# Kernel optimization log

Measured on AMD Instinct MI355X. Metric: run time of the kernel, lower is better.

## Reference

```python
import jax, jax.numpy as jnp
import numpy as np

# Dims: B=1, S=2048, D=1024, L=4 blocks, INNER=2*D=2048, NH=4 heads (DH=512),
# conv K=4, qkv blocksize BS=4 (NB=512 block-diagonal blocks).

def _ln(x, w, eps=1e-5):
    mu = x.mean(-1, keepdims=True)
    var = x.var(-1, keepdims=True)
    return (x - mu) * jax.lax.rsqrt(var + eps) * w


def setup_inputs() -> dict:
    key = jax.random.key(0)
    B, S, D = 1, 2048, 1024
    L, NH, K, BS = 4, 4, 4, 4
    INNER = 2 * D
    NB = INNER // BS
    ks = iter(jax.random.split(key, 40))
    rn = lambda *sh: jax.random.normal(next(ks), sh, jnp.float32) * 0.02
    return dict(
        tokens_batch=jax.random.normal(next(ks), (B, S, D), jnp.float32),
        ln_w=jnp.ones((L, D), jnp.float32),
        up_w=rn(L, 2 * INNER, D),
        conv_w=rn(L, INNER, K),
        conv_b=jnp.zeros((L, INNER), jnp.float32),
        q_w=rn(L, NB, BS, BS),
        k_w=rn(L, NB, BS, BS),
        v_w=rn(L, NB, BS, BS),
        ig_w=rn(L, NH, 3 * INNER),
        ig_b=jnp.zeros((L, NH), jnp.float32),
        fg_w=rn(L, NH, 3 * INNER),
        fg_b=jnp.tile(jnp.linspace(3.0, 6.0, NH, dtype=jnp.float32), (L, 1)),
        skip=jnp.ones((L, INNER), jnp.float32),
        onorm_w=jnp.ones((L, INNER), jnp.float32),
        down_w=rn(L, D, INNER),
        post_w=jnp.ones((D,), jnp.float32),
        lat_w=rn(32 * 32, D), lat_b=jnp.zeros((32 * 32,), jnp.float32),
        r1_w=rn(D, D), r1_b=jnp.zeros((D,), jnp.float32),
        r2_w=rn(1, D), r2_b=jnp.zeros((1,), jnp.float32),
        t1_w=rn(D, D), t1_b=jnp.zeros((D,), jnp.float32),
        t2_w=rn(1, D), t2_b=jnp.zeros((1,), jnp.float32),
    )


def reference(tokens_batch, ln_w, up_w, conv_w, conv_b, q_w, k_w, v_w,
              ig_w, ig_b, fg_w, fg_b, skip, onorm_w, down_w, post_w,
              lat_w, lat_b, r1_w, r1_b, r2_w, r2_b, t1_w, t1_b, t2_w, t2_b):
    B, S, D = tokens_batch.shape
    L, INNER, K = conv_w.shape
    NH = ig_w.shape[1]
    DH = INNER // NH
    NB, BS = q_w.shape[1], q_w.shape[2]
    mask = jnp.tril(jnp.ones((S, S), bool))
    x = tokens_batch
    for l in range(L):
        xn = _ln(x, ln_w[l])                                  # pre-LN (weight only)
        up = jnp.einsum('bsd,ed->bse', xn, up_w[l])           # (B,S,2*INNER)
        xm, z = up[..., :INNER], up[..., INNER:]
        # causal depthwise conv1d + swish
        xp = jnp.pad(xm, ((0, 0), (K - 1, 0), (0, 0)))
        xc = conv_b[l] + sum(xp[:, k:k + S, :] * conv_w[l, :, k] for k in range(K))
        xc = jax.nn.silu(xc)
        # block-diagonal (headwise) q/k/v projections
        def headwise(inp, w):
            return jnp.einsum('bsnd,nod->bsno', inp.reshape(B, S, NB, BS), w).reshape(B, S, INNER)
        q = headwise(xc, q_w[l]); kk = headwise(xc, k_w[l]); v = headwise(xm, v_w[l])
        gin = jnp.concatenate([q, kk, v], axis=-1)            # (B,S,3*INNER)
        ig = (jnp.einsum('bse,he->bsh', gin, ig_w[l]) + ig_b[l]).transpose(0, 2, 1)  # (B,NH,S)
        fg = (jnp.einsum('bse,he->bsh', gin, fg_w[l]) + fg_b[l]).transpose(0, 2, 1)
        qh = q.reshape(B, S, NH, DH).transpose(0, 2, 1, 3)
        kh = kk.reshape(B, S, NH, DH).transpose(0, 2, 1, 3)
        vh = v.reshape(B, S, NH, DH).transpose(0, 2, 1, 3)
        # parallel stabilized mLSTM (rowwise stabilization)
        cs = jnp.cumsum(jax.nn.log_sigmoid(fg), axis=-1)      # (B,NH,S)
        logD = jnp.where(mask, cs[..., :, None] - cs[..., None, :], -jnp.inf) + ig[:, :, None, :]
        m = jnp.max(logD, axis=-1, keepdims=True)
        Dm = jnp.exp(logD - m)
        qk = jnp.einsum('bhsd,bhtd->bhst', qh, kh) / jnp.sqrt(jnp.float32(DH))
        C = qk * Dm
        n = jnp.maximum(jnp.abs(C.sum(-1, keepdims=True)), jnp.exp(-m))
        h = jnp.einsum('bhst,bhtd->bhsd', C / (n + 1e-6), vh)
        # multi-head layernorm over DH per head, then channel scale
        ht = h.transpose(0, 2, 1, 3)                           # (B,S,NH,DH)
        mu = ht.mean(-1, keepdims=True); var = ht.var(-1, keepdims=True)
        ht = (ht - mu) * jax.lax.rsqrt(var + 1e-5) * onorm_w[l].reshape(NH, DH)
        ht = ht.reshape(B, S, INNER) + skip[l] * xc            # learnable skip
        out = ht * jax.nn.silu(z)                              # output gate
        x = x + jnp.einsum('bse,de->bsd', out, down_w[l])      # residual
    x = _ln(x, post_w)
    latent = jnp.einsum('bsd,ed->bse', x, lat_w) + lat_b
    reward = jnp.einsum('bsd,ed->bse', jnp.einsum('bsd,ed->bse', x, r1_w) + r1_b, r2_w) + r2_b
    term = jnp.einsum('bsd,ed->bse', jnp.einsum('bsd,ed->bse', x, t1_w) + t1_b, t2_w) + t2_b
    return (latent, reward, term)
```

## Files before the change

### kernel.cpp

```cpp
#include <hip/hip_runtime.h>
#include <hip/hip_bf16.h>
#include <math.h>
#include <cstdint>

typedef __bf16 bf16_t;
typedef bf16_t bf16x8 __attribute__((ext_vector_type(8)));
typedef bf16_t bf16x4 __attribute__((ext_vector_type(4)));
typedef bf16_t bf16x2 __attribute__((ext_vector_type(2)));
typedef float f32x4 __attribute__((ext_vector_type(4)));
typedef float f32x2 __attribute__((ext_vector_type(2)));

#define S_LEN 2048
#define DMODEL 1024
#define NLAYER 4
#define NHEAD 4
#define INNER 2048
#define DHEAD 512
#define NBLK 512
#define UPCOLS 4096
#define GIN 6144

#define GLDS16(gp, lp)                                              \
  __builtin_amdgcn_global_load_lds(                                 \
      (const __attribute__((address_space(1))) void*)(gp),          \
      (__attribute__((address_space(3))) void*)(lp), 16, 0, 0)

__global__ __launch_bounds__(256) void cvt_f32_bf16(const float* __restrict__ in,
                                                    bf16_t* __restrict__ out, int n4) {
  int i = blockIdx.x * 256 + threadIdx.x;
  int stride = gridDim.x * 256;
  for (; i < n4; i += stride) {
    f32x4 v = ((const f32x4*)in)[i];
    bf16x4 o;
    #pragma unroll
    for (int j = 0; j < 4; j++) o[j] = (bf16_t)v[j];
    ((bf16x4*)out)[i] = o;
  }
}

__global__ __launch_bounds__(256) void ln_fused(const float* src, const float* p0,
                                                const float* p1, const float* __restrict__ w,
                                                float* Xout, bf16_t* __restrict__ out) {
  int s = blockIdx.x;
  int t = threadIdx.x;
  size_t base = (size_t)s * DMODEL;
  f32x4 v = ((const f32x4*)(src + base))[t];
  if (p0) {
    f32x4 a = ((const f32x4*)(p0 + base))[t];
    f32x4 b = ((const f32x4*)(p1 + base))[t];
    #pragma unroll
    for (int j = 0; j < 4; j++) v[j] += a[j] + b[j];
  }
  ((f32x4*)(Xout + base))[t] = v;
  float s1 = v[0] + v[1] + v[2] + v[3];
  float s2 = v[0]*v[0] + v[1]*v[1] + v[2]*v[2] + v[3]*v[3];
  __shared__ float b1[4], b2[4];
  #pragma unroll
  for (int off = 32; off; off >>= 1) { s1 += __shfl_xor(s1, off); s2 += __shfl_xor(s2, off); }
  if ((t & 63) == 0) { b1[t >> 6] = s1; b2[t >> 6] = s2; }
  __syncthreads();
  float tot1 = b1[0] + b1[1] + b1[2] + b1[3];
  float tot2 = b2[0] + b2[1] + b2[2] + b2[3];
  float mu = tot1 * (1.f / DMODEL);
  float var = tot2 * (1.f / DMODEL) - mu * mu;
  float rs = rsqrtf(var + 1e-5f);
  bf16x4 o;
  #pragma unroll
  for (int j = 0; j < 4; j++) o[j] = (bf16_t)((v[j] - mu) * rs * w[t * 4 + j]);
  ((bf16x4*)(out + base))[t] = o;
}

__global__ __launch_bounds__(256) void conv_qkv_kernel(
    const float* __restrict__ UP, const float* __restrict__ cw, const float* __restrict__ cb,
    const float* __restrict__ qw, const float* __restrict__ kw, const float* __restrict__ vw,
    float* __restrict__ XC, bf16_t* __restrict__ Q, bf16_t* __restrict__ Kb, bf16_t* __restrict__ V) {
  int s = blockIdx.y;
  int n = blockIdx.x * 256 + threadIdx.x;
  int c0 = n * 4;
  f32x4 zero4 = {};
  f32x4 xm[4];
  #pragma unroll
  for (int k = 0; k < 4; k++) {
    int sr = s + k - 3;
    xm[k] = (sr >= 0) ? *(const f32x4*)(UP + (size_t)sr * UPCOLS + c0) : zero4;
  }
  f32x4 cbv = *(const f32x4*)(cb + c0);
  float xc[4];
  #pragma unroll
  for (int d = 0; d < 4; d++) {
    f32x4 wv = *(const f32x4*)(cw + (size_t)(c0 + d) * 4);
    float a = cbv[d];
    #pragma unroll
    for (int k = 0; k < 4; k++) a += wv[k] * xm[k][d];
    xc[d] = a / (1.f + __expf(-a));
  }
  f32x4 xcv; xcv[0]=xc[0]; xcv[1]=xc[1]; xcv[2]=xc[2]; xcv[3]=xc[3];
  *(f32x4*)(XC + (size_t)s * INNER + c0) = xcv;
  bf16x4 qo, ko, vo;
  #pragma unroll
  for (int o = 0; o < 4; o++) {
    float aq = 0, ak = 0, av = 0;
    #pragma unroll
    for (int d = 0; d < 4; d++) {
      aq += qw[n * 16 + o * 4 + d] * xc[d];
      ak += kw[n * 16 + o * 4 + d] * xc[d];
      av += vw[n * 16 + o * 4 + d] * xm[3][d];
    }
    qo[o] = (bf16_t)aq; ko[o] = (bf16_t)ak; vo[o] = (bf16_t)av;
  }
  ((bf16x4*)(Q  + (size_t)s * INNER))[n] = qo;
  ((bf16x4*)(Kb + (size_t)s * INNER))[n] = ko;
  ((bf16x4*)(V  + (size_t)s * INNER))[n] = vo;
}

__global__ __launch_bounds__(256) void transpose_bf16(const bf16_t* __restrict__ in,
                                                      bf16_t* __restrict__ out) {
  __shared__ bf16_t tile[32][33];
  int c0 = blockIdx.x * 32, r0 = blockIdx.y * 32;
  int tx = threadIdx.x & 31, ty = threadIdx.x >> 5;
  #pragma unroll
  for (int i = ty; i < 32; i += 8) tile[i][tx] = in[(size_t)(r0 + i) * INNER + c0 + tx];
  __syncthreads();
  #pragma unroll
  for (int i = ty; i < 32; i += 8) out[(size_t)(c0 + i) * S_LEN + r0 + tx] = tile[tx][i];
}

__global__ __launch_bounds__(256) void gates_kernel(
    const bf16_t* __restrict__ Q, const bf16_t* __restrict__ K, const bf16_t* __restrict__ V,
    const float* __restrict__ igw, const float* __restrict__ igb,
    const float* __restrict__ fgw, const float* __restrict__ fgb,
    float* __restrict__ IG, float* __restrict__ FG) {
  int s = blockIdx.x;
  float pi[NHEAD] = {0, 0, 0, 0}, pf[NHEAD] = {0, 0, 0, 0};
  for (int e = threadIdx.x; e < GIN; e += 256) {
    float g;
    if (e < INNER)            g = (float)Q[(size_t)s * INNER + e];
    else if (e < 2 * INNER)   g = (float)K[(size_t)s * INNER + e - INNER];
    else                      g = (float)V[(size_t)s * INNER + e - 2 * INNER];
    #pragma unroll
    for (int h = 0; h < NHEAD; h++) {
      pi[h] += g * igw[h * GIN + e];
      pf[h] += g * fgw[h * GIN + e];
    }
  }
  __shared__ float red[8][4];
  #pragma unroll
  for (int h = 0; h < NHEAD; h++) {
    float a = pi[h], b = pf[h];
    #pragma unroll
    for (int off = 32; off; off >>= 1) { a += __shfl_xor(a, off); b += __shfl_xor(b, off); }
    if ((threadIdx.x & 63) == 0) { red[h][threadIdx.x >> 6] = a; red[h + 4][threadIdx.x >> 6] = b; }
  }
  __syncthreads();
  if (threadIdx.x < NHEAD) {
    int h = threadIdx.x;
    IG[h * S_LEN + s] = red[h][0] + red[h][1] + red[h][2] + red[h][3] + igb[h];
    FG[h * S_LEN + s] = red[h + 4][0] + red[h + 4][1] + red[h + 4][2] + red[h + 4][3] + fgb[h];
  }
}

__global__ __launch_bounds__(256) void scan_kernel(const float* __restrict__ IG,
                                                   const float* __restrict__ FG,
                                                   float* __restrict__ AV, float* __restrict__ PM,
                                                   float* __restrict__ NF, float* __restrict__ NRAW) {
  int h = blockIdx.x;
  int tid = threadIdx.x;
  const float* fg = FG + h * S_LEN;
  const float* ig = IG + h * S_LEN;
  float cs[8];
  float run = 0.f;
  #pragma unroll
  for (int i = 0; i < 8; i++) {
    float x = fg[tid * 8 + i];
    float l = (x >= 0.f) ? -log1pf(__expf(-x)) : (x - log1pf(__expf(x)));
    run += l; cs[i] = run;
  }
  __shared__ float sb[256];
  sb[tid] = run;
  __syncthreads();
  for (int off = 1; off < 256; off <<= 1) {
    float add = (tid >= off) ? sb[tid - off] : 0.f;
    __syncthreads();
    sb[tid] += add;
    __syncthreads();
  }
  float base = sb[tid] - run;
  float a[8];
  float runm = -__builtin_inff();
  #pragma unroll
  for (int i = 0; i < 8; i++) {
    cs[i] += base;
    a[i] = ig[tid * 8 + i] - cs[i];
    runm = fmaxf(runm, a[i]);
  }
  __syncthreads();
  sb[tid] = runm;
  __syncthreads();
  for (int off = 1; off < 256; off <<= 1) {
    float other = (tid >= off) ? sb[tid - off] : -__builtin_inff();
    __syncthreads();
    sb[tid] = fmaxf(sb[tid], other);
    __syncthreads();
  }
  float rm = (tid == 0) ? -__builtin_inff() : sb[tid - 1];
  #pragma unroll
  for (int i = 0; i < 8; i++) {
    rm = fmaxf(rm, a[i]);
    AV[h * S_LEN + tid * 8 + i] = a[i];
    PM[h * S_LEN + tid * 8 + i] = rm;
    NF[h * S_LEN + tid * 8 + i] = __expf(-(cs[i] + rm));
    NRAW[h * S_LEN + tid * 8 + i] = 0.f;
  }
}

__global__ void scale_kernel(const float* __restrict__ nraw, const float* __restrict__ nf,
                             float* __restrict__ scale, int n) {
  int i = blockIdx.x * 256 + threadIdx.x;
  if (i < n) scale[i] = 1.f / (fmaxf(fabsf(nraw[i]), nf[i]) + 1e-6f);
}

__global__ __launch_bounds__(256) void onorm_kernel(
    const float* __restrict__ Hp0, const float* __restrict__ Hp1,
    const float* __restrict__ XC, const float* __restrict__ UP,
    const float* __restrict__ onw, const float* __restrict__ skipw, bf16_t* __restrict__ OUT) {
  int h = blockIdx.x, s = blockIdx.y;
  int c = h * DHEAD + threadIdx.x * 2;
  size_t idx = (size_t)s * INNER + c;
  f32x2 v0 = *(const f32x2*)(Hp0 + idx);
  f32x2 v1 = *(const f32x2*)(Hp1 + idx);
  f32x2 v; v[0] = v0[0] + v1[0]; v[1] = v0[1] + v1[1];
  float s1 = v[0] + v[1], s2 = v[0] * v[0] + v[1] * v[1];
  __shared__ float b1[4], b2[4];
  #pragma unroll
  for (int off = 32; off; off >>= 1) { s1 += __shfl_xor(s1, off); s2 += __shfl_xor(s2, off); }
  if ((threadIdx.x & 63) == 0) { b1[threadIdx.x >> 6] = s1; b2[threadIdx.x >> 6] = s2; }
  __syncthreads();
  float tot1 = b1[0] + b1[1] + b1[2] + b1[3];
  float tot2 = b2[0] + b2[1] + b2[2] + b2[3];
  float mu = tot1 * (1.f / DHEAD);
  float var = tot2 * (1.f / DHEAD) - mu * mu;
  float rs = rsqrtf(var + 1e-5f);
  bf16x2 o;
  #pragma unroll
  for (int j = 0; j < 2; j++) {
    float val = (v[j] - mu) * rs * onw[c + j] + skipw[c + j] * XC[idx + j];
    float z = UP[(size_t)s * UPCOLS + INNER + c + j];
    val *= z / (1.f + __expf(-z));
    o[j] = (bf16_t)val;
  }
  *(bf16x2*)(OUT + idx) = o;
}

__global__ __launch_bounds__(256) void latcopy_kernel(const float* __restrict__ Ch,
                                                      const float* __restrict__ b,
                                                      float* __restrict__ out) {
  int s = blockIdx.x, t = threadIdx.x;
  f32x4 v = ((const f32x4*)(Ch + (size_t)s * 3072))[t];
  f32x4 bb = ((const f32x4*)b)[t];
  f32x4 o; o[0]=v[0]+bb[0]; o[1]=v[1]+bb[1]; o[2]=v[2]+bb[2]; o[3]=v[3]+bb[3];
  ((f32x4*)(out + (size_t)s * DMODEL))[t] = o;
}

__global__ __launch_bounds__(256) void rt_kernel(
    const float* __restrict__ Ch,
    const float* __restrict__ r1b, const float* __restrict__ t1b,
    const float* __restrict__ r2w, const float* __restrict__ r2b,
    const float* __restrict__ t2w, const float* __restrict__ t2b,
    float* __restrict__ outR, float* __restrict__ outT) {
  int s = blockIdx.x, t = threadIdx.x;
  f32x4 a = ((const f32x4*)(Ch + (size_t)s * 3072 + 1024))[t];
  f32x4 b = ((const f32x4*)(Ch + (size_t)s * 3072 + 2048))[t];
  f32x4 ab = ((const f32x4*)r1b)[t];
  f32x4 bb = ((const f32x4*)t1b)[t];
  f32x4 w1 = ((const f32x4*)r2w)[t];
  f32x4 w2 = ((const f32x4*)t2w)[t];
  float pr = 0, pt = 0;
  #pragma unroll
  for (int j = 0; j < 4; j++) {
    pr += (a[j] + ab[j]) * w1[j];
    pt += (b[j] + bb[j]) * w2[j];
  }
  __shared__ float rb[4], tb[4];
  #pragma unroll
  for (int off = 32; off; off >>= 1) { pr += __shfl_xor(pr, off); pt += __shfl_xor(pt, off); }
  if ((t & 63) == 0) { rb[t >> 6] = pr; tb[t >> 6] = pt; }
  __syncthreads();
  if (t == 0) {
    outR[s] = rb[0] + rb[1] + rb[2] + rb[3] + r2b[0];
    outT[s] = tb[0] + tb[1] + tb[2] + tb[3] + t2b[0];
  }
}

#define BM 128
#define BN 128

template <int MODE>
__global__ __launch_bounds__(256) void gemm_kernel(
    const bf16_t* __restrict__ A, int lda, long long sAz,
    const bf16_t* __restrict__ B, int ldb, long long sBz,
    float* __restrict__ C, int ldc, long long sCz,
    bf16_t* __restrict__ P, long long sPz,
    int K,
    const float* __restrict__ avec, const float* __restrict__ pmvec,
    float* __restrict__ nraw,
    const float* __restrict__ scalev, long long sVz) {
  int gx = gridDim.x, gxy = gx * gridDim.y;
  int nwg = gxy * gridDim.z;
  int orig = blockIdx.z * gxy + blockIdx.y * gx + blockIdx.x;
  int xcd = orig & 7, lo = orig >> 3;
  int q8 = nwg >> 3, r8 = nwg & 7;
  int wg = (xcd < r8 ? xcd * (q8 + 1) : r8 * (q8 + 1) + (xcd - r8) * q8) + lo;
  int z = wg / gxy; int rem = wg - z * gxy;
  int by, bx;
  if (MODE == 3) {
    by = (int)((sqrtf(8.f * (float)rem + 1.f) - 1.f) * 0.5f);
    while ((by + 1) * (by + 2) / 2 <= rem) by++;
    while (by * (by + 1) / 2 > rem) by--;
    bx = rem - by * (by + 1) / 2;
  } else {
    by = rem / gx; bx = rem - by * gx;
  }
  int m0 = by * BM;
  int n0 = bx * BN;

  int head = z, kbeg = 0, kend = K;
  if (MODE == 4) {
    head = z >> 1;
    int kf = m0 + BM; if (kf > K) kf = K;
    int half = kf >> 1;
    kbeg = (z & 1) * half; kend = kbeg + half;
    A += (size_t)head * sAz; B += (size_t)head * sBz;
  } else if (MODE == 6) {
    head = 0;
    int half = K >> 1;
    kbeg = z * half; kend = kbeg + half;
  } else {
    A += (size_t)z * sAz; B += (size_t)z * sBz;
  }
  int nt = (kend - kbeg) >> 5;

  __shared__ __align__(16) bf16_t smem[32768];

  int tid = threadIdx.x;
  int lane = tid & 63;
  int wave = tid >> 6;
  int wr = wave >> 1, wc = wave & 1;
  int l15 = lane & 15, lk = lane >> 4;

  int csw = ((lane & 3) ^ ((lane >> 3) & 3)) * 8;
  const bf16_t* pA0 = A + (size_t)(m0 + wave * 32 + (lane >> 2)) * lda + kbeg + csw;
  const bf16_t* pA1 = pA0 + (size_t)16 * lda;
  const bf16_t* pB0 = B + (size_t)(n0 + wave * 32 + (lane >> 2)) * ldb + kbeg + csw;
  const bf16_t* pB1 = pB0 + (size_t)16 * ldb;

#define STAGE(t)                                       \
  do {                                                 \
    int _ko = (t) * 32;                                \
    bf16_t* _b = smem + ((t) & 3) * 8192 + wave * 1024;\
    GLDS16(pA0 + _ko, _b);                             \
    GLDS16(pA1 + _ko, _b + 512);                       \
    GLDS16(pB0 + _ko, _b + 4096);                      \
    GLDS16(pB1 + _ko, _b + 4096 + 512);                \
  } while (0)

  int aoff[4], boff[4];
  #pragma unroll
  for (int m = 0; m < 4; m++) {
    int ra = wr * 64 + m * 16 + l15;
    aoff[m] = ra * 64 + ((lk ^ ((ra >> 1) & 3)) * 16);
    int rb = wc * 64 + m * 16 + l15;
    boff[m] = 8192 + rb * 64 + ((lk ^ ((rb >> 1) & 3)) * 16);
  }

  f32x4 acc[4][4] = {};

  int npre = nt < 3 ? nt : 3;
  for (int s = 0; s < npre; ++s) STAGE(s);

  for (int t = 0; t < nt; ++t) {
    int remt = nt - 1 - t;
    if (remt >= 2)      asm volatile("s_waitcnt vmcnt(8)" ::: "memory");
    else if (remt == 1) asm volatile("s_waitcnt vmcnt(4)" ::: "memory");
    else                asm volatile("s_waitcnt vmcnt(0)" ::: "memory");
    __builtin_amdgcn_s_barrier();
    if (t + 3 < nt) STAGE(t + 3);
    const char* base = (const char*)smem + (t & 3) * 16384;
    bf16x8 af[4], bfv[4];
    #pragma unroll
    for (int m = 0; m < 4; m++) af[m] = *(const bf16x8*)(base + aoff[m]);
    #pragma unroll
    for (int n = 0; n < 4; n++) bfv[n] = *(const bf16x8*)(base + boff[n]);
    asm volatile("s_waitcnt lgkmcnt(0)" ::: "memory");
    __builtin_amdgcn_sched_barrier(0);
    __builtin_amdgcn_s_setprio(1);
    #pragma unroll
    for (int m = 0; m < 4; m++)
      #pragma unroll
      for (int n = 0; n < 4; n++)
        acc[m][n] = __builtin_amdgcn_mfma_f32_16x16x32_bf16(af[m], bfv[n], acc[m][n], 0, 0, 0);
    __builtin_amdgcn_s_setprio(0);
  }
#undef STAGE

  int rbase = m0 + wr * 64;
  int cbase = n0 + wc * 64;
  if (MODE == 3) {
    __syncthreads();
    const float* av = avec + z * sVz;
    const float* pv = pmvec + z * sVz;
    float* nr = nraw + z * sVz;
    bf16_t* Pp = P + z * sPz;
    const float ISQ = 0.04419417382415922f;
    #pragma unroll
    for (int m = 0; m < 4; m++) {
      float rsum[4] = {0, 0, 0, 0};
      #pragma unroll
      for (int n = 0; n < 4; n++) {
        int cg = cbase + n * 16 + l15;
        float aexp = av[cg];
        #pragma unroll
        for (int r = 0; r < 4; r++) {
          int rg = rbase + m * 16 + lk * 4 + r;
          float val = 0.f;
          if (cg <= rg) val = acc[m][n][r] * ISQ * __expf(aexp - pv[rg]);
          smem[(size_t)(wr * 64 + m * 16 + lk * 4 + r) * 136 + wc * 64 + n * 16 + l15] =
              (bf16_t)val;
          rsum[r] += val;
        }
      }
      #pragma unroll
      for (int r = 0; r < 4; r++) {
        float v = rsum[r];
        v += __shfl_xor(v, 1); v += __shfl_xor(v, 2); v += __shfl_xor(v, 4); v += __shfl_xor(v, 8);
        if (l15 == 0) atomicAdd(&nr[rbase + m * 16 + lk * 4 + r], v);
      }
    }
    __syncthreads();
    #pragma unroll
    for (int i = 0; i < 8; i++) {
      int chunk = tid + i * 256;
      int row = chunk >> 4, cc = chunk & 15;
      *(bf16x8*)(Pp + (size_t)(m0 + row) * ldc + n0 + cc * 8) =
          *(const bf16x8*)(smem + (size_t)row * 136 + cc * 8);
    }
  } else {
    float* Cp = C;
    if (MODE == 4) Cp = C + (size_t)head * sCz + (size_t)(z & 1) * sPz;
    else if (MODE == 6) Cp = C + (size_t)z * sPz;
    else Cp = C + (size_t)head * sCz;
    #pragma unroll
    for (int m = 0; m < 4; m++) {
      #pragma unroll
      for (int r = 0; r < 4; r++) {
        int rg = rbase + m * 16 + lk * 4 + r;
        float rowscale = (MODE == 4) ? scalev[head * sVz + rg] : 1.f;
        #pragma unroll
        for (int n = 0; n < 4; n++) {
          int cg = cbase + n * 16 + l15;
          size_t idx = (size_t)rg * ldc + cg;
          float v = acc[m][n][r];
          if (MODE == 4) Cp[idx] = v * rowscale;
          else Cp[idx] = v;
        }
      }
    }
  }
}

extern "C" void kernel_launch(void* const* d_in, const int* in_sizes, int n_in,
                              void* d_out, int out_size, void* d_ws, size_t ws_size,
                              hipStream_t stream) {
  const float* tokens = (const float*)d_in[0];
  const float* ln_w   = (const float*)d_in[1];
  const float* up_w   = (const float*)d_in[2];
  const float* conv_w = (const float*)d_in[3];
  const float* conv_b = (const float*)d_in[4];
  const float* q_w    = (const float*)d_in[5];
  const float* k_w    = (const float*)d_in[6];
  const float* v_w    = (const float*)d_in[7];
  const float* ig_w   = (const float*)d_in[8];
  const float* ig_b   = (const float*)d_in[9];
  const float* fg_w   = (const float*)d_in[10];
  const float* fg_b   = (const float*)d_in[11];
  const float* skipw  = (const float*)d_in[12];
  const float* onormw = (const float*)d_in[13];
  const float* down_w = (const float*)d_in[14];
  const float* post_w = (const float*)d_in[15];
  const float* lat_w  = (const float*)d_in[16];
  const float* lat_b  = (const float*)d_in[17];
  const float* r1_w   = (const float*)d_in[18];
  const float* r1_b   = (const float*)d_in[19];
  const float* r2_w   = (const float*)d_in[20];
  const float* r2_b   = (const float*)d_in[21];
  const float* t1_w   = (const float*)d_in[22];
  const float* t1_b   = (const float*)d_in[23];
  const float* t2_w   = (const float*)d_in[24];
  const float* t2_b   = (const float*)d_in[25];

  char* ws = (char*)d_ws;
  size_t off = 0;
  auto alloc = [&](size_t bytes) -> char* {
    char* p = ws + off;
    off += (bytes + 255) & ~(size_t)255;
    return p;
  };
  float*  X    = (float*)alloc((size_t)S_LEN * DMODEL * 4);
  float*  UP   = (float*)alloc((size_t)S_LEN * UPCOLS * 4);
  float*  XC   = (float*)alloc((size_t)S_LEN * INNER * 4);
  float*  Hp0  = (float*)alloc((size_t)S_LEN * INNER * 4);
  float*  Hp1  = (float*)alloc((size_t)S_LEN * INNER * 4);
  bf16_t* XN   = (bf16_t*)alloc((size_t)S_LEN * DMODEL * 2);
  bf16_t* Qb   = (bf16_t*)alloc((size_t)S_LEN * INNER * 2);
  bf16_t* Kb   = (bf16_t*)alloc((size_t)S_LEN * INNER * 2);
  bf16_t* Vb   = (bf16_t*)alloc((size_t)S_LEN * INNER * 2);
  bf16_t* VT   = (bf16_t*)alloc((size_t)S_LEN * INNER * 2);
  bf16_t* Pb   = (bf16_t*)alloc((size_t)NHEAD * S_LEN * S_LEN * 2);
  bf16_t* OUTb = (bf16_t*)alloc((size_t)S_LEN * INNER * 2);
  bf16_t* WbU  = (bf16_t*)alloc((size_t)NLAYER * UPCOLS * DMODEL * 2);
  bf16_t* WbD  = (bf16_t*)alloc((size_t)NLAYER * DMODEL * INNER * 2);
  bf16_t* Wh   = (bf16_t*)alloc((size_t)3 * DMODEL * DMODEL * 2);
  float*  IG   = (float*)alloc(NHEAD * S_LEN * 4);
  float*  FG   = (float*)alloc(NHEAD * S_LEN * 4);
  float*  AV   = (float*)alloc(NHEAD * S_LEN * 4);
  float*  PM   = (float*)alloc(NHEAD * S_LEN * 4);
  float*  NF   = (float*)alloc(NHEAD * S_LEN * 4);
  float*  NRAW = (float*)alloc(NHEAD * S_LEN * 4);
  float*  SCL  = (float*)alloc(NHEAD * S_LEN * 4);
  float* Dp0 = Hp0;
  float* Dp1 = Hp0 + (size_t)S_LEN * DMODEL;
  float* Chead = UP;
  float* latent_out = (float*)d_out;
  float* reward_out = (float*)d_out + (size_t)S_LEN * DMODEL;
  float* term_out   = reward_out + S_LEN;

  if (off > ws_size) return;

  cvt_f32_bf16<<<2048, 256, 0, stream>>>(up_w, WbU, NLAYER * UPCOLS * DMODEL / 4);
  cvt_f32_bf16<<<1024, 256, 0, stream>>>(down_w, WbD, NLAYER * DMODEL * INNER / 4);
  cvt_f32_bf16<<<512, 256, 0, stream>>>(lat_w, Wh, DMODEL * DMODEL / 4);
  cvt_f32_bf16<<<512, 256, 0, stream>>>(r1_w, Wh + (size_t)DMODEL * DMODEL, DMODEL * DMODEL / 4);
  cvt_f32_bf16<<<512, 256, 0, stream>>>(t1_w, Wh + 2 * (size_t)DMODEL * DMODEL,
                                        DMODEL * DMODEL / 4);

  for (int l = 0; l < NLAYER; l++) {
    ln_fused<<<S_LEN, 256, 0, stream>>>(l == 0 ? tokens : X, l == 0 ? nullptr : Dp0,
                                        l == 0 ? nullptr : Dp1, ln_w + l * DMODEL, X, XN);
    gemm_kernel<0><<<dim3(UPCOLS / BN, S_LEN / BM, 1), 256, 0, stream>>>(
        XN, DMODEL, 0, WbU + (size_t)l * UPCOLS * DMODEL, DMODEL, 0, UP, UPCOLS, 0, nullptr, 0,
        DMODEL, nullptr, nullptr, nullptr, nullptr, 0);
    conv_qkv_kernel<<<dim3(2, S_LEN), 256, 0, stream>>>(
        UP, conv_w + (size_t)l * INNER * 4, conv_b + l * INNER,
        q_w + (size_t)l * NBLK * 16, k_w + (size_t)l * NBLK * 16, v_w + (size_t)l * NBLK * 16,
        XC, Qb, Kb, Vb);
    transpose_bf16<<<dim3(64, 64), 256, 0, stream>>>(Vb, VT);
    gates_kernel<<<S_LEN, 256, 0, stream>>>(Qb, Kb, Vb, ig_w + (size_t)l * NHEAD * GIN,
                                            ig_b + l * NHEAD, fg_w + (size_t)l * NHEAD * GIN,
                                            fg_b + l * NHEAD, IG, FG);
    scan_kernel<<<NHEAD, 256, 0, stream>>>(IG, FG, AV, PM, NF, NRAW);
    gemm_kernel<3><<<dim3(136, 1, NHEAD), 256, 0, stream>>>(
        Qb, INNER, DHEAD, Kb, INNER, DHEAD, nullptr, S_LEN, 0, Pb, (long long)S_LEN * S_LEN,
        DHEAD, AV, PM, NRAW, nullptr, S_LEN);
    scale_kernel<<<(NHEAD * S_LEN + 255) / 256, 256, 0, stream>>>(NRAW, NF, SCL, NHEAD * S_LEN);
    gemm_kernel<4><<<dim3(DHEAD / BN, S_LEN / BM, 2 * NHEAD), 256, 0, stream>>>(
        Pb, S_LEN, (long long)S_LEN * S_LEN, VT, S_LEN, (long long)DHEAD * S_LEN,
        Hp0, INNER, DHEAD, nullptr, (long long)S_LEN * INNER,
        S_LEN, nullptr, nullptr, nullptr, SCL, S_LEN);
    onorm_kernel<<<dim3(NHEAD, S_LEN), 256, 0, stream>>>(Hp0, Hp1, XC, UP, onormw + l * INNER,
                                                         skipw + l * INNER, OUTb);
    gemm_kernel<6><<<dim3(DMODEL / BN, S_LEN / BM, 2), 256, 0, stream>>>(
        OUTb, INNER, 0, WbD + (size_t)l * DMODEL * INNER, INNER, 0, Dp0, DMODEL, 0, nullptr,
        (long long)S_LEN * DMODEL, INNER, nullptr, nullptr, nullptr, nullptr, 0);
  }

  ln_fused<<<S_LEN, 256, 0, stream>>>(X, Dp0, Dp1, post_w, X, XN);
  gemm_kernel<0><<<dim3(3072 / BN, S_LEN / BM, 1), 256, 0, stream>>>(
      XN, DMODEL, 0, Wh, DMODEL, 0, Chead, 3072, 0, nullptr, 0,
      DMODEL, nullptr, nullptr, nullptr, nullptr, 0);
  latcopy_kernel<<<S_LEN, 256, 0, stream>>>(Chead, lat_b, latent_out);
  rt_kernel<<<S_LEN, 256, 0, stream>>>(Chead, r1_b, t1_b, r2_w, r2_b, t2_w, t2_b,
                                       reward_out, term_out);
}
```

Before: 977.7 us.

## Switch GEMM to 256x256 tiles with 512 threads and double buffering

Every GEMM mode now uses 256x256 output tiles computed by 8 waves (512 threads), each wave holding an 8x4 MFMA accumulator block. The 4-deep LDS pipeline becomes a double buffer with an extra barrier per k-step. The down-projection GEMM's split-K goes from 2 to 4, so the LayerNorm kernel now sums four partial outputs. The aim is more operand reuse per LDS load and fewer workgroups. The cost is much lower parallelism: the triangular QK kernel drops to 36 blocks per head and the up GEMM to 128 blocks on a 256-CU part. It also means higher register pressure, a shallower prefetch, and a two-pass staged P epilogue.

```diff
diff --git a/kernel.cpp b/kernel.cpp
--- a/kernel.cpp
+++ b/kernel.cpp
@@ -39,7 +39,8 @@
 }
 
 __global__ __launch_bounds__(256) void ln_fused(const float* src, const float* p0,
-                                                const float* p1, const float* __restrict__ w,
+                                                const float* p1, const float* p2,
+                                                const float* p3, const float* __restrict__ w,
                                                 float* Xout, bf16_t* __restrict__ out) {
   int s = blockIdx.x;
   int t = threadIdx.x;
@@ -48,8 +49,10 @@
   if (p0) {
     f32x4 a = ((const f32x4*)(p0 + base))[t];
     f32x4 b = ((const f32x4*)(p1 + base))[t];
-    #pragma unroll
-    for (int j = 0; j < 4; j++) v[j] += a[j] + b[j];
+    f32x4 c = ((const f32x4*)(p2 + base))[t];
+    f32x4 d = ((const f32x4*)(p3 + base))[t];
+    #pragma unroll
+    for (int j = 0; j < 4; j++) v[j] += (a[j] + b[j]) + (c[j] + d[j]);
   }
   ((f32x4*)(Xout + base))[t] = v;
   float s1 = v[0] + v[1] + v[2] + v[3];
@@ -291,11 +294,9 @@
   }
 }
 
-#define BM 128
-#define BN 128
 
 template <int MODE>
-__global__ __launch_bounds__(256) void gemm_kernel(
+__global__ __launch_bounds__(512) void gemm_kernel(
     const bf16_t* __restrict__ A, int lda, long long sAz,
     const bf16_t* __restrict__ B, int ldb, long long sBz,
     float* __restrict__ C, int ldc, long long sCz,
@@ -320,20 +321,20 @@
   } else {
     by = rem / gx; bx = rem - by * gx;
   }
-  int m0 = by * BM;
-  int n0 = bx * BN;
+  int m0 = by * 256;
+  int n0 = bx * 256;
 
   int head = z, kbeg = 0, kend = K;
   if (MODE == 4) {
     head = z >> 1;
-    int kf = m0 + BM; if (kf > K) kf = K;
+    int kf = m0 + 256; if (kf > K) kf = K;
     int half = kf >> 1;
     kbeg = (z & 1) * half; kend = kbeg + half;
     A += (size_t)head * sAz; B += (size_t)head * sBz;
   } else if (MODE == 6) {
     head = 0;
-    int half = K >> 1;
-    kbeg = z * half; kend = kbeg + half;
+    int quarter = K >> 2;
+    kbeg = z * quarter; kend = kbeg + quarter;
   } else {
     A += (size_t)z * sAz; B += (size_t)z * sBz;
   }
@@ -344,57 +345,62 @@
   int tid = threadIdx.x;
   int lane = tid & 63;
   int wave = tid >> 6;
-  int wr = wave >> 1, wc = wave & 1;
+  int wr = wave >> 2;
+  int wc = wave & 3;
   int l15 = lane & 15, lk = lane >> 4;
 
-  int csw = ((lane & 3) ^ ((lane >> 3) & 3)) * 8;
-  const bf16_t* pA0 = A + (size_t)(m0 + wave * 32 + (lane >> 2)) * lda + kbeg + csw;
-  const bf16_t* pA1 = pA0 + (size_t)16 * lda;
-  const bf16_t* pB0 = B + (size_t)(n0 + wave * 32 + (lane >> 2)) * ldb + kbeg + csw;
-  const bf16_t* pB1 = pB0 + (size_t)16 * ldb;
-
-#define STAGE(t)                                       \
+  int row0 = tid >> 2;
+  int csw = ((tid & 3) ^ ((row0 >> 1) & 3)) * 8;
+  const bf16_t* pA0 = A + (size_t)(m0 + row0) * lda + kbeg + csw;
+  const bf16_t* pA1 = pA0 + (size_t)128 * lda;
+  const bf16_t* pB0 = B + (size_t)(n0 + row0) * ldb + kbeg + csw;
+  const bf16_t* pB1 = pB0 + (size_t)128 * ldb;
+
+#define STAGE(t, db)                                   \
   do {                                                 \
     int _ko = (t) * 32;                                \
-    bf16_t* _b = smem + ((t) & 3) * 8192 + wave * 1024;\
+    bf16_t* _b = smem + (db) * 16384 + wave * 512;     \
     GLDS16(pA0 + _ko, _b);                             \
-    GLDS16(pA1 + _ko, _b + 512);                       \
-    GLDS16(pB0 + _ko, _b + 4096);                      \
-    GLDS16(pB1 + _ko, _b + 4096 + 512);                \
+    GLDS16(pA1 + _ko, _b + 4096);                      \
+    GLDS16(pB0 + _ko, _b + 8192);                      \
+    GLDS16(pB1 + _ko, _b + 12288);                     \
   } while (0)
 
-  int aoff[4], boff[4];
-  #pragma unroll
-  for (int m = 0; m < 4; m++) {
-    int ra = wr * 64 + m * 16 + l15;
+  int aoff[8], boff[4];
+  #pragma unroll
+  for (int m = 0; m < 8; m++) {
+    int ra = wr * 128 + m * 16 + l15;
     aoff[m] = ra * 64 + ((lk ^ ((ra >> 1) & 3)) * 16);
-    int rb = wc * 64 + m * 16 + l15;
-    boff[m] = 8192 + rb * 64 + ((lk ^ ((rb >> 1) & 3)) * 16);
-  }
-
-  f32x4 acc[4][4] = {};
-
-  int npre = nt < 3 ? nt : 3;
-  for (int s = 0; s < npre; ++s) STAGE(s);
-
+  }
+  #pragma unroll
+  for (int n = 0; n < 4; n++) {
+    int rb = wc * 64 + n * 16 + l15;
+    boff[n] = 16384 + rb * 64 + ((lk ^ ((rb >> 1) & 3)) * 16);
+  }
+
+  f32x4 acc[8][4] = {};
+
+  STAGE(0, 0);
   for (int t = 0; t < nt; ++t) {
-    int remt = nt - 1 - t;
-    if (remt >= 2)      asm volatile("s_waitcnt vmcnt(8)" ::: "memory");
-    else if (remt == 1) asm volatile("s_waitcnt vmcnt(4)" ::: "memory");
-    else                asm volatile("s_waitcnt vmcnt(0)" ::: "memory");
     __builtin_amdgcn_s_barrier();
-    if (t + 3 < nt) STAGE(t + 3);
-    const char* base = (const char*)smem + (t & 3) * 16384;
-    bf16x8 af[4], bfv[4];
-    #pragma unroll
-    for (int m = 0; m < 4; m++) af[m] = *(const bf16x8*)(base + aoff[m]);
+    if (t + 1 < nt) {
+      STAGE(t + 1, (t + 1) & 1);
+      asm volatile("s_waitcnt vmcnt(4)" ::: "memory");
+    } else {
+      asm volatile("s_waitcnt vmcnt(0)" ::: "memory");
+    }
+    __builtin_amdgcn_s_barrier();
+    const char* base = (const char*)smem + (t & 1) * 32768;
+    bf16x8 af[8], bfv[4];
+    #pragma unroll
+    for (int m = 0; m < 8; m++) af[m] = *(const bf16x8*)(base + aoff[m]);
     #pragma unroll
     for (int n = 0; n < 4; n++) bfv[n] = *(const bf16x8*)(base + boff[n]);
     asm volatile("s_waitcnt lgkmcnt(0)" ::: "memory");
     __builtin_amdgcn_sched_barrier(0);
     __builtin_amdgcn_s_setprio(1);
     #pragma unroll
-    for (int m = 0; m < 4; m++)
+    for (int m = 0; m < 8; m++)
       #pragma unroll
       for (int n = 0; n < 4; n++)
         acc[m][n] = __builtin_amdgcn_mfma_f32_16x16x32_bf16(af[m], bfv[n], acc[m][n], 0, 0, 0);
@@ -402,54 +408,63 @@
   }
 #undef STAGE
 
-  int rbase = m0 + wr * 64;
+  int rbase = m0 + wr * 128;
   int cbase = n0 + wc * 64;
   if (MODE == 3) {
-    __syncthreads();
     const float* av = avec + z * sVz;
     const float* pv = pmvec + z * sVz;
     float* nr = nraw + z * sVz;
     bf16_t* Pp = P + z * sPz;
     const float ISQ = 0.04419417382415922f;
     #pragma unroll
-    for (int m = 0; m < 4; m++) {
-      float rsum[4] = {0, 0, 0, 0};
-      #pragma unroll
-      for (int n = 0; n < 4; n++) {
-        int cg = cbase + n * 16 + l15;
-        float aexp = av[cg];
+    for (int half = 0; half < 2; half++) {
+      __syncthreads();
+      if ((wc >> 1) == half) {
         #pragma unroll
-        for (int r = 0; r < 4; r++) {
-          int rg = rbase + m * 16 + lk * 4 + r;
-          float val = 0.f;
-          if (cg <= rg) val = acc[m][n][r] * ISQ * __expf(aexp - pv[rg]);
-          smem[(size_t)(wr * 64 + m * 16 + lk * 4 + r) * 136 + wc * 64 + n * 16 + l15] =
-              (bf16_t)val;
-          rsum[r] += val;
+        for (int m = 0; m < 8; m++) {
+          float rsum[4] = {0, 0, 0, 0};
+          #pragma unroll
+          for (int n = 0; n < 4; n++) {
+            int cg = cbase + n * 16 + l15;
+            int colin = (wc & 1) * 64 + n * 16 + l15;
+            float aexp = av[cg];
+            #pragma unroll
+            for (int r = 0; r < 4; r++) {
+              int rowin = wr * 128 + m * 16 + lk * 4 + r;
+              int rg = m0 + rowin;
+              float val = 0.f;
+              if (cg <= rg) val = acc[m][n][r] * ISQ * __expf(aexp - pv[rg]);
+              int slot = (colin >> 3) ^ (rowin & 15);
+              *(bf16_t*)((char*)smem + rowin * 256 + slot * 16 + (colin & 7) * 2) =
+                  (bf16_t)val;
+              rsum[r] += val;
+            }
+          }
+          #pragma unroll
+          for (int r = 0; r < 4; r++) {
+            float v = rsum[r];
+            v += __shfl_xor(v, 1); v += __shfl_xor(v, 2);
+            v += __shfl_xor(v, 4); v += __shfl_xor(v, 8);
+            if (l15 == 0) atomicAdd(&nr[rbase + m * 16 + lk * 4 + r], v);
+          }
         }
       }
+      __syncthreads();
       #pragma unroll
-      for (int r = 0; r < 4; r++) {
-        float v = rsum[r];
-        v += __shfl_xor(v, 1); v += __shfl_xor(v, 2); v += __shfl_xor(v, 4); v += __shfl_xor(v, 8);
-        if (l15 == 0) atomicAdd(&nr[rbase + m * 16 + lk * 4 + r], v);
+      for (int i = 0; i < 8; i++) {
+        int idx = tid + i * 512;
+        int row = idx >> 4, cc = idx & 15;
+        int slot = cc ^ (row & 15);
+        *(bf16x8*)(Pp + (size_t)(m0 + row) * ldc + n0 + half * 128 + cc * 8) =
+            *(const bf16x8*)((const char*)smem + row * 256 + slot * 16);
       }
-    }
-    __syncthreads();
-    #pragma unroll
-    for (int i = 0; i < 8; i++) {
-      int chunk = tid + i * 256;
-      int row = chunk >> 4, cc = chunk & 15;
-      *(bf16x8*)(Pp + (size_t)(m0 + row) * ldc + n0 + cc * 8) =
-          *(const bf16x8*)(smem + (size_t)row * 136 + cc * 8);
     }
   } else {
     float* Cp = C;
     if (MODE == 4) Cp = C + (size_t)head * sCz + (size_t)(z & 1) * sPz;
     else if (MODE == 6) Cp = C + (size_t)z * sPz;
-    else Cp = C + (size_t)head * sCz;
-    #pragma unroll
-    for (int m = 0; m < 4; m++) {
+    #pragma unroll
+    for (int m = 0; m < 8; m++) {
       #pragma unroll
       for (int r = 0; r < 4; r++) {
         int rg = rbase + m * 16 + lk * 4 + r;
@@ -528,6 +543,8 @@
   float*  SCL  = (float*)alloc(NHEAD * S_LEN * 4);
   float* Dp0 = Hp0;
   float* Dp1 = Hp0 + (size_t)S_LEN * DMODEL;
+  float* Dp2 = Hp0 + 2 * (size_t)S_LEN * DMODEL;
+  float* Dp3 = Hp0 + 3 * (size_t)S_LEN * DMODEL;
   float* Chead = UP;
   float* latent_out = (float*)d_out;
   float* reward_out = (float*)d_out + (size_t)S_LEN * DMODEL;
@@ -544,8 +561,9 @@
 
   for (int l = 0; l < NLAYER; l++) {
     ln_fused<<<S_LEN, 256, 0, stream>>>(l == 0 ? tokens : X, l == 0 ? nullptr : Dp0,
-                                        l == 0 ? nullptr : Dp1, ln_w + l * DMODEL, X, XN);
-    gemm_kernel<0><<<dim3(UPCOLS / BN, S_LEN / BM, 1), 256, 0, stream>>>(
+                                        l == 0 ? nullptr : Dp1, l == 0 ? nullptr : Dp2,
+                                        l == 0 ? nullptr : Dp3, ln_w + l * DMODEL, X, XN);
+    gemm_kernel<0><<<dim3(UPCOLS / 256, S_LEN / 256, 1), 512, 0, stream>>>(
         XN, DMODEL, 0, WbU + (size_t)l * UPCOLS * DMODEL, DMODEL, 0, UP, UPCOLS, 0, nullptr, 0,
         DMODEL, nullptr, nullptr, nullptr, nullptr, 0);
     conv_qkv_kernel<<<dim3(2, S_LEN), 256, 0, stream>>>(
@@ -557,23 +575,23 @@
                                             ig_b + l * NHEAD, fg_w + (size_t)l * NHEAD * GIN,
                                             fg_b + l * NHEAD, IG, FG);
     scan_kernel<<<NHEAD, 256, 0, stream>>>(IG, FG, AV, PM, NF, NRAW);
-    gemm_kernel<3><<<dim3(136, 1, NHEAD), 256, 0, stream>>>(
+    gemm_kernel<3><<<dim3(36, 1, NHEAD), 512, 0, stream>>>(
         Qb, INNER, DHEAD, Kb, INNER, DHEAD, nullptr, S_LEN, 0, Pb, (long long)S_LEN * S_LEN,
         DHEAD, AV, PM, NRAW, nullptr, S_LEN);
     scale_kernel<<<(NHEAD * S_LEN + 255) / 256, 256, 0, stream>>>(NRAW, NF, SCL, NHEAD * S_LEN);
-    gemm_kernel<4><<<dim3(DHEAD / BN, S_LEN / BM, 2 * NHEAD), 256, 0, stream>>>(
+    gemm_kernel<4><<<dim3(DHEAD / 256, S_LEN / 256, 2 * NHEAD), 512, 0, stream>>>(
         Pb, S_LEN, (long long)S_LEN * S_LEN, VT, S_LEN, (long long)DHEAD * S_LEN,
         Hp0, INNER, DHEAD, nullptr, (long long)S_LEN * INNER,
         S_LEN, nullptr, nullptr, nullptr, SCL, S_LEN);
     onorm_kernel<<<dim3(NHEAD, S_LEN), 256, 0, stream>>>(Hp0, Hp1, XC, UP, onormw + l * INNER,
                                                          skipw + l * INNER, OUTb);
-    gemm_kernel<6><<<dim3(DMODEL / BN, S_LEN / BM, 2), 256, 0, stream>>>(
+    gemm_kernel<6><<<dim3(DMODEL / 256, S_LEN / 256, 4), 512, 0, stream>>>(
         OUTb, INNER, 0, WbD + (size_t)l * DMODEL * INNER, INNER, 0, Dp0, DMODEL, 0, nullptr,
         (long long)S_LEN * DMODEL, INNER, nullptr, nullptr, nullptr, nullptr, 0);
   }
 
-  ln_fused<<<S_LEN, 256, 0, stream>>>(X, Dp0, Dp1, post_w, X, XN);
-  gemm_kernel<0><<<dim3(3072 / BN, S_LEN / BM, 1), 256, 0, stream>>>(
+  ln_fused<<<S_LEN, 256, 0, stream>>>(X, Dp0, Dp1, Dp2, Dp3, post_w, X, XN);
+  gemm_kernel<0><<<dim3(3072 / 256, S_LEN / 256, 1), 512, 0, stream>>>(
       XN, DMODEL, 0, Wh, DMODEL, 0, Chead, 3072, 0, nullptr, 0,
       DMODEL, nullptr, nullptr, nullptr, nullptr, 0);
   latcopy_kernel<<<S_LEN, 256, 0, stream>>>(Chead, lat_b, latent_out);
```

New measurement: 1.210 ms. 1.24x slower.
